# Kernel optimization log

Measured on AMD Instinct MI355X. Metric: run time of the kernel, lower is better.

Reference implementation:

```python
import jax, jax.numpy as jnp
import numpy as np

EPS = 1e-6
K_STEPS = 4
USE_GATING = True


def layer_norm(x, gamma, beta):
    mu = jnp.mean(x, axis=-1, keepdims=True)
    var = jnp.mean(jnp.square(x - mu), axis=-1, keepdims=True)
    return (x - mu) * jax.lax.rsqrt(var + EPS) * gamma + beta


def setup_inputs() -> dict:
    key = jax.random.key(0)
    B, L, D, H = 4, 4096, 2048, 8192
    ks = jax.random.split(key, 16)
    s = 0.02
    return {
        "x": jax.random.normal(ks[0], (B, L, D), dtype=jnp.float32),
        "in_gamma": jnp.ones((D,), jnp.float32),
        "in_beta": jnp.zeros((D,), jnp.float32),
        "agg_w": jax.random.normal(ks[1], (D, D), jnp.float32) * s,
        "agg_b": jnp.zeros((D,), jnp.float32),
        "pn_gamma": jnp.ones((D,), jnp.float32),
        "pn_beta": jnp.zeros((D,), jnp.float32),
        "d1_w": jax.random.normal(ks[2], (D, H), jnp.float32) * s,
        "d1_b": jnp.zeros((H,), jnp.float32),
        "d2_w": jax.random.normal(ks[3], (H, D), jnp.float32) * s,
        "d2_b": jnp.zeros((D,), jnp.float32),
        "bc_w": jax.random.normal(ks[4], (D, D), jnp.float32) * s,
        "bc_b": jnp.zeros((D,), jnp.float32),
        "gate_w": jax.random.normal(ks[5], (D, D), jnp.float32) * s,
        "gate_b": jnp.zeros((D,), jnp.float32),
        "out_gamma": jnp.ones((D,), jnp.float32),
        "out_beta": jnp.zeros((D,), jnp.float32),
    }


def reference(x, in_gamma, in_beta, agg_w, agg_b, pn_gamma, pn_beta,
              d1_w, d1_b, d2_w, d2_b, bc_w, bc_b, gate_w, gate_b,
              out_gamma, out_beta):
    # Input norm over the full sequence, then extract last-position summary.
    x_norm = layer_norm(x, in_gamma, in_beta)              # [B, L, D]
    thought = x_norm[:, -1, :] @ agg_w + agg_b             # [B, D]

    # Iterative pre-norm MLP thought refinement (fixed small k -> unrolled).
    for _ in range(K_STEPS):
        t = layer_norm(thought, pn_gamma, pn_beta)
        t = jax.nn.gelu(t @ d1_w + d1_b, approximate=False)
        thought = thought + (t @ d2_w + d2_b)

    # Broadcast refined thought back to every position.
    broadcast = (thought @ bc_w + bc_b)[:, None, :]        # [B, 1, D]

    if USE_GATING:
        gate = jax.nn.sigmoid(x @ gate_w + gate_b)         # [B, L, D]
        out = x + gate * broadcast
    else:
        out = x + broadcast
    return layer_norm(out, out_gamma, out_beta)
```

## Files before the change

kernel.cpp:

```cpp
#include <hip/hip_runtime.h>
#include <stdint.h>

typedef __attribute__((ext_vector_type(8))) short short8;
typedef __attribute__((ext_vector_type(4))) float f32x4;
typedef __attribute__((ext_vector_type(4))) unsigned short us4;

__device__ inline unsigned short f2bf(float f) {
    unsigned u = __float_as_uint(f);
    u = (u + 0x7FFFu + ((u >> 16) & 1u)) >> 16;
    return (unsigned short)u;
}

__device__ inline float bf2f(unsigned short u) {
    return __uint_as_float(((unsigned)u) << 16);
}

__device__ inline float gelu_f(float v) {
    return 0.5f * v * (1.0f + erff(v * 0.70710678118654752f));
}

__device__ inline void gload_lds16(const unsigned short* g, const unsigned short* l) {
    __builtin_amdgcn_global_load_lds(
        (const __attribute__((address_space(1))) unsigned int*)(g),
        (__attribute__((address_space(3))) unsigned int*)(l),
        16, 0, 0);
}

__global__ __launch_bounds__(256) void cvt_x_kernel(const float* __restrict__ in,
                                                    unsigned short* __restrict__ out, int n4) {
    int i = blockIdx.x * 256 + threadIdx.x;
    if (i >= n4) return;
    float4 v = reinterpret_cast<const float4*>(in)[i];
    us4 o = { f2bf(v.x), f2bf(v.y), f2bf(v.z), f2bf(v.w) };
    reinterpret_cast<us4*>(out)[i] = o;
}

__global__ __launch_bounds__(256) void transpose_w_kernel(const float* __restrict__ W,
                                                          unsigned short* __restrict__ WT,
                                                          int K, int N) {
    __shared__ float tile[32][33];
    int bn = blockIdx.x * 32;
    int bk = blockIdx.y * 32;
    int tx = threadIdx.x & 31;
    int ty = threadIdx.x >> 5;
#pragma unroll
    for (int j = 0; j < 32; j += 8)
        tile[ty + j][tx] = W[(long long)(bk + ty + j) * N + bn + tx];
    __syncthreads();
#pragma unroll
    for (int j = 0; j < 32; j += 8)
        WT[(long long)(bn + ty + j) * K + bk + tx] = f2bf(tile[tx][ty + j]);
}

__device__ inline void block_reduce2(float& s, float& q) {
#pragma unroll
    for (int o = 32; o > 0; o >>= 1) {
        s += __shfl_xor(s, o, 64);
        q += __shfl_xor(q, o, 64);
    }
    __shared__ float sh[8];
    __syncthreads();
    int w = threadIdx.x >> 6;
    if ((threadIdx.x & 63) == 0) { sh[w] = s; sh[4 + w] = q; }
    __syncthreads();
    s = (sh[0] + sh[1]) + (sh[2] + sh[3]);
    q = (sh[4] + sh[5]) + (sh[6] + sh[7]);
}

__global__ __launch_bounds__(256) void ln_rows_kernel(const float* __restrict__ in, long long in_stride,
                                                      float* __restrict__ out, long long out_stride,
                                                      const float* __restrict__ gamma,
                                                      const float* __restrict__ beta) {
    const float* p = in + (long long)blockIdx.x * in_stride;
    float* q = out + (long long)blockIdx.x * out_stride;
    int t = threadIdx.x;
    float4 a = reinterpret_cast<const float4*>(p)[t];
    float4 c = reinterpret_cast<const float4*>(p)[t + 256];
    float s  = (a.x + a.y) + (a.z + a.w) + (c.x + c.y) + (c.z + c.w);
    float ss = a.x*a.x + a.y*a.y + a.z*a.z + a.w*a.w
             + c.x*c.x + c.y*c.y + c.z*c.z + c.w*c.w;
    block_reduce2(s, ss);
    const float inv = 1.0f / 2048.0f;
    float mu = s * inv;
    float var = ss * inv - mu * mu;
    float rs = rsqrtf(var + 1e-6f);
    float4 g0 = reinterpret_cast<const float4*>(gamma)[t];
    float4 g1 = reinterpret_cast<const float4*>(gamma)[t + 256];
    float4 b0 = reinterpret_cast<const float4*>(beta)[t];
    float4 b1 = reinterpret_cast<const float4*>(beta)[t + 256];
    float4 o0, o1;
    o0.x = (a.x - mu) * rs * g0.x + b0.x;
    o0.y = (a.y - mu) * rs * g0.y + b0.y;
    o0.z = (a.z - mu) * rs * g0.z + b0.z;
    o0.w = (a.w - mu) * rs * g0.w + b0.w;
    o1.x = (c.x - mu) * rs * g1.x + b1.x;
    o1.y = (c.y - mu) * rs * g1.y + b1.y;
    o1.z = (c.z - mu) * rs * g1.z + b1.z;
    o1.w = (c.w - mu) * rs * g1.w + b1.w;
    reinterpret_cast<float4*>(q)[t] = o0;
    reinterpret_cast<float4*>(q)[t + 256] = o1;
}

template<int MODE>
__global__ __launch_bounds__(256) void gemv4f_kernel(const float* __restrict__ src, long long sstride,
                                                     const float* __restrict__ gamma,
                                                     const float* __restrict__ beta,
                                                     const float* __restrict__ W,
                                                     const float* __restrict__ bias,
                                                     float* __restrict__ out,
                                                     int K, int N, int KC) {
    __shared__ float sA[4][128];
    const int tid = threadIdx.x;
    const int k0 = blockIdx.y * KC;

    float mu[4], rsd[4];
    if (MODE == 1) {
#pragma unroll
        for (int r = 0; r < 4; ++r) {
            const float* p = src + r * sstride;
            float s = 0.f, q = 0.f;
            for (int k = tid; k < K; k += 256) { float v = p[k]; s += v; q += v * v; }
            block_reduce2(s, q);
            float m = s / K;
            mu[r] = m;
            rsd[r] = rsqrtf(q / K - m * m + 1e-6f);
        }
    }
    for (int idx = tid; idx < 4 * KC; idx += 256) {
        int r = idx / KC, k = idx - r * KC;
        float v = src[r * sstride + k0 + k];
        if (MODE == 1) v = (v - mu[r]) * rsd[r] * gamma[k0 + k] + beta[k0 + k];
        if (MODE == 2) v = gelu_f(v);
        sA[r][k] = v;
    }
    __syncthreads();

    const int n4 = blockIdx.x * 256 + tid;
    const int n = n4 * 4;
    const float4* W4 = reinterpret_cast<const float4*>(W);
    float4 a0 = {0.f, 0.f, 0.f, 0.f}, a1 = a0, a2 = a0, a3 = a0;
#pragma unroll 4
    for (int k = 0; k < KC; ++k) {
        float4 w = W4[((long long)(k0 + k) * N + n) >> 2];
        float c0 = sA[0][k], c1 = sA[1][k], c2 = sA[2][k], c3 = sA[3][k];
        a0.x = fmaf(c0, w.x, a0.x); a0.y = fmaf(c0, w.y, a0.y);
        a0.z = fmaf(c0, w.z, a0.z); a0.w = fmaf(c0, w.w, a0.w);
        a1.x = fmaf(c1, w.x, a1.x); a1.y = fmaf(c1, w.y, a1.y);
        a1.z = fmaf(c1, w.z, a1.z); a1.w = fmaf(c1, w.w, a1.w);
        a2.x = fmaf(c2, w.x, a2.x); a2.y = fmaf(c2, w.y, a2.y);
        a2.z = fmaf(c2, w.z, a2.z); a2.w = fmaf(c2, w.w, a2.w);
        a3.x = fmaf(c3, w.x, a3.x); a3.y = fmaf(c3, w.y, a3.y);
        a3.z = fmaf(c3, w.z, a3.z); a3.w = fmaf(c3, w.w, a3.w);
    }
    if (blockIdx.y == 0) {
        float4 b = reinterpret_cast<const float4*>(bias)[n4];
        a0.x += b.x; a0.y += b.y; a0.z += b.z; a0.w += b.w;
        a1.x += b.x; a1.y += b.y; a1.z += b.z; a1.w += b.w;
        a2.x += b.x; a2.y += b.y; a2.z += b.z; a2.w += b.w;
        a3.x += b.x; a3.y += b.y; a3.z += b.z; a3.w += b.w;
    }
    atomicAdd(&out[n + 0], a0.x); atomicAdd(&out[n + 1], a0.y);
    atomicAdd(&out[n + 2], a0.z); atomicAdd(&out[n + 3], a0.w);
    atomicAdd(&out[N + n + 0], a1.x); atomicAdd(&out[N + n + 1], a1.y);
    atomicAdd(&out[N + n + 2], a1.z); atomicAdd(&out[N + n + 3], a1.w);
    atomicAdd(&out[2 * N + n + 0], a2.x); atomicAdd(&out[2 * N + n + 1], a2.y);
    atomicAdd(&out[2 * N + n + 2], a2.z); atomicAdd(&out[2 * N + n + 3], a2.w);
    atomicAdd(&out[3 * N + n + 0], a3.x); atomicAdd(&out[3 * N + n + 1], a3.y);
    atomicAdd(&out[3 * N + n + 2], a3.z); atomicAdd(&out[3 * N + n + 3], a3.w);
}

#define BK 64
__global__ __launch_bounds__(512, 2) void gate_gemm_kernel(const unsigned short* __restrict__ A,
                                                           const unsigned short* __restrict__ BT,
                                                           const float* __restrict__ gate_b,
                                                           const float* __restrict__ bcast,
                                                           float* __restrict__ pre,
                                                           int M, int N, int K) {
    extern __shared__ unsigned short lds[];
    const int tid = threadIdx.x;
    const int lane = tid & 63;
    const int wave = tid >> 6;
    const int wm = wave >> 2;
    const int wn = wave & 3;
    const int bm0 = blockIdx.x * 256;
    const int bn0 = blockIdx.y * 256;
    const int NT = K / BK;

    const int ch0 = wave * 64 + lane;
    const int ch1 = 512 + wave * 64 + lane;
    const int r0 = ch0 >> 3, c0s = (ch0 & 7) ^ (r0 & 7);
    const int r1 = ch1 >> 3, c1s = (ch1 & 7) ^ (r1 & 7);
    const int srcoff0 = r0 * K + c0s * 8;
    const int srcoff1 = r1 * K + c1s * 8;
    const int ldso0 = ch0 * 8;
    const int ldso1 = ch1 * 8;

    const unsigned short* Abase = A + (long long)bm0 * K;
    const unsigned short* Bbase = BT + (long long)bn0 * K;

#define STAGE_A(buf, h, t)  do { \
        const unsigned short* g = Abase + (h) * 128 * K + (t) * BK; \
        const unsigned short* d = &lds[(buf) * 16384 + (h) * 8192]; \
        gload_lds16(g + srcoff0, d + ldso0); \
        gload_lds16(g + srcoff1, d + ldso1); } while (0)
#define STAGE_B(buf, h, t)  do { \
        const unsigned short* g = Bbase + (h) * 128 * K + (t) * BK; \
        const unsigned short* d = &lds[32768 + (buf) * 16384 + (h) * 8192]; \
        gload_lds16(g + srcoff0, d + ldso0); \
        gload_lds16(g + srcoff1, d + ldso1); } while (0)

    f32x4 acc[8][4];
#pragma unroll
    for (int i = 0; i < 8; ++i)
#pragma unroll
        for (int j = 0; j < 4; ++j)
#pragma unroll
            for (int r = 0; r < 4; ++r) acc[i][j][r] = 0.f;

    const int r16 = lane & 15, kq = lane >> 4;

    STAGE_A(0, 0, 0); STAGE_A(0, 1, 0);
    STAGE_B(0, 0, 0); STAGE_B(0, 1, 0);
    asm volatile("s_waitcnt vmcnt(0)" ::: "memory");
    __builtin_amdgcn_s_barrier();

    for (int t = 0; t < NT; ++t) {
        const int p = t & 1;
        const int u = t + 1;
        const int a_base = p * 16384 + wm * 8192;
        const int b_base = 32768 + p * 16384 + (wn >> 1) * 8192;

        if (u < NT) {
            STAGE_A(1 - p, 0, u); STAGE_A(1 - p, 1, u);
            STAGE_B(1 - p, 0, u); STAGE_B(1 - p, 1, u);
        }
        __builtin_amdgcn_sched_barrier(0);

        short8 bf[4][2];
#pragma unroll
        for (int ni = 0; ni < 4; ++ni) {
            const int rl = (wn & 1) * 64 + ni * 16 + r16;
#pragma unroll
            for (int kk = 0; kk < 2; ++kk)
                bf[ni][kk] = *reinterpret_cast<const short8*>(
                    &lds[b_base + rl * 64 + (((kk << 2) | kq) ^ (rl & 7)) * 8]);
        }
#pragma unroll
        for (int mh = 0; mh < 2; ++mh) {
            short8 af[4][2];
#pragma unroll
            for (int mi = 0; mi < 4; ++mi) {
                const int rl = mh * 64 + mi * 16 + r16;
#pragma unroll
                for (int kk = 0; kk < 2; ++kk)
                    af[mi][kk] = *reinterpret_cast<const short8*>(
                        &lds[a_base + rl * 64 + (((kk << 2) | kq) ^ (rl & 7)) * 8]);
            }
            __builtin_amdgcn_s_setprio(1);
#pragma unroll
            for (int mi = 0; mi < 4; ++mi)
#pragma unroll
                for (int ni = 0; ni < 4; ++ni)
#pragma unroll
                    for (int kk = 0; kk < 2; ++kk)
                        acc[mh * 4 + mi][ni] = __builtin_amdgcn_mfma_f32_16x16x32_bf16(
                            af[mi][kk], bf[ni][kk], acc[mh * 4 + mi][ni], 0, 0, 0);
            __builtin_amdgcn_s_setprio(0);
        }
        asm volatile("s_waitcnt vmcnt(0)" ::: "memory");
        __builtin_amdgcn_s_barrier();
    }

    const int bnum = bm0 >> 12;
    const float* bc_row = bcast + (long long)bnum * N;
#pragma unroll
    for (int mi = 0; mi < 8; ++mi) {
        const int row = bm0 + wm * 128 + mi * 16 + kq * 4;
#pragma unroll
        for (int ni = 0; ni < 4; ++ni) {
            const int col = bn0 + wn * 64 + ni * 16 + r16;
            const float gb = gate_b[col];
            const float bc = bc_row[col];
#pragma unroll
            for (int r = 0; r < 4; ++r) {
                const long long off = (long long)(row + r) * N + col;
                const float v = acc[mi][ni][r] + gb;
                const float g = 1.0f / (1.0f + __expf(-v));
                pre[off] = bf2f(A[off]) + g * bc;
            }
        }
    }
}
#undef STAGE_A
#undef STAGE_B

extern "C" void kernel_launch(void* const* d_in, const int* in_sizes, int n_in,
                              void* d_out, int out_size, void* d_ws, size_t ws_size,
                              hipStream_t stream) {
    const float* x         = (const float*)d_in[0];
    const float* in_gamma  = (const float*)d_in[1];
    const float* in_beta   = (const float*)d_in[2];
    const float* agg_w     = (const float*)d_in[3];
    const float* agg_b     = (const float*)d_in[4];
    const float* pn_gamma  = (const float*)d_in[5];
    const float* pn_beta   = (const float*)d_in[6];
    const float* d1_w      = (const float*)d_in[7];
    const float* d1_b      = (const float*)d_in[8];
    const float* d2_w      = (const float*)d_in[9];
    const float* d2_b      = (const float*)d_in[10];
    const float* bc_w      = (const float*)d_in[11];
    const float* bc_b      = (const float*)d_in[12];
    const float* gate_w    = (const float*)d_in[13];
    const float* gate_b    = (const float*)d_in[14];
    const float* out_gamma = (const float*)d_in[15];
    const float* out_beta  = (const float*)d_in[16];

    const int B = 4, L = 4096, D = 2048, H = 8192;
    const int M = B * L;
    float* out = (float*)d_out;

    char* ws = (char*)d_ws;
    unsigned short* xb  = (unsigned short*)ws;
    unsigned short* gwT = (unsigned short*)(ws + 67108864);
    float* tbuf  = (float*)(ws + 75497472);
    float* bcast = tbuf + 4 * D;
    float* hbuf0 = bcast + 4 * D;

    static bool attr_done = false;
    if (!attr_done) {
        hipFuncSetAttribute((const void*)gate_gemm_kernel,
                            hipFuncAttributeMaxDynamicSharedMemorySize, 131072);
        attr_done = true;
    }

    hipMemsetAsync(tbuf, 0, (4 * D + 4 * D + 4 * 4 * H) * sizeof(float), stream);

    gemv4f_kernel<1><<<dim3(D / 1024, 64), dim3(256), 0, stream>>>(
        x + (long long)(L - 1) * D, (long long)L * D, in_gamma, in_beta,
        agg_w, agg_b, tbuf, D, D, 32);

    for (int s = 0; s < 4; ++s) {
        float* hbuf = hbuf0 + s * 4 * H;
        gemv4f_kernel<1><<<dim3(H / 1024, 32), dim3(256), 0, stream>>>(
            tbuf, (long long)D, pn_gamma, pn_beta, d1_w, d1_b, hbuf, D, H, 64);
        gemv4f_kernel<2><<<dim3(D / 1024, 128), dim3(256), 0, stream>>>(
            hbuf, (long long)H, nullptr, nullptr, d2_w, d2_b, tbuf, H, D, 64);
    }
    gemv4f_kernel<0><<<dim3(D / 1024, 64), dim3(256), 0, stream>>>(
        tbuf, (long long)D, nullptr, nullptr, bc_w, bc_b, bcast, D, D, 32);

    cvt_x_kernel<<<dim3((M * D / 4) / 256), dim3(256), 0, stream>>>(x, xb, M * D / 4);
    transpose_w_kernel<<<dim3(D / 32, D / 32), dim3(256), 0, stream>>>(gate_w, gwT, D, D);

    gate_gemm_kernel<<<dim3(M / 256, D / 256), dim3(512), 131072, stream>>>(
        xb, gwT, gate_b, bcast, out, M, D, D);

    ln_rows_kernel<<<dim3(M), dim3(256), 0, stream>>>(
        out, (long long)D, out, (long long)D, out_gamma, out_beta);
}
```

Baseline: 525.8 us.

## Shrink gate GEMM tile to 128x128 and swap grid order for N-fastest traversal

Reduces the gate GEMM block tile from 256x256 to 128x128 with 512 threads. Each wave now computes a 64x32 sub-tile, LDS drops to 64KB, and launch bounds allow 4 blocks per CU. The grid is reordered so blockIdx.x walks N, which means consecutive blocks share the same A rows. The intent is higher occupancy and better latency hiding, paid for by lower arithmetic intensity per tile and more global and LDS traffic per FLOP.

```diff
diff --git a/kernel.cpp b/kernel.cpp
--- a/kernel.cpp
+++ b/kernel.cpp
@@ -170,7 +170,7 @@
 }
 
 #define BK 64
-__global__ __launch_bounds__(512, 2) void gate_gemm_kernel(const unsigned short* __restrict__ A,
+__global__ __launch_bounds__(512, 4) void gate_gemm_kernel(const unsigned short* __restrict__ A,
                                                            const unsigned short* __restrict__ BT,
                                                            const float* __restrict__ gate_b,
                                                            const float* __restrict__ bcast,
@@ -182,12 +182,11 @@
     const int wave = tid >> 6;
     const int wm = wave >> 2;
     const int wn = wave & 3;
-    const int bm0 = blockIdx.x * 256;
-    const int bn0 = blockIdx.y * 256;
+    const int bn0 = blockIdx.x * 128;
+    const int bm0 = blockIdx.y * 128;
     const int NT = K / BK;
 
-    const int ch0 = wave * 64 + lane;
-    const int ch1 = 512 + wave * 64 + lane;
+    const int ch0 = tid, ch1 = tid + 512;
     const int r0 = ch0 >> 3, c0s = (ch0 & 7) ^ (r0 & 7);
     const int r1 = ch1 >> 3, c1s = (ch1 & 7) ^ (r1 & 7);
     const int srcoff0 = r0 * K + c0s * 8;
@@ -198,75 +197,68 @@
     const unsigned short* Abase = A + (long long)bm0 * K;
     const unsigned short* Bbase = BT + (long long)bn0 * K;
 
-#define STAGE_A(buf, h, t)  do { \
-        const unsigned short* g = Abase + (h) * 128 * K + (t) * BK; \
-        const unsigned short* d = &lds[(buf) * 16384 + (h) * 8192]; \
+#define STAGE_A(buf, t)  do { \
+        const unsigned short* g = Abase + (t) * BK; \
+        const unsigned short* d = &lds[(buf) * 8192]; \
         gload_lds16(g + srcoff0, d + ldso0); \
         gload_lds16(g + srcoff1, d + ldso1); } while (0)
-#define STAGE_B(buf, h, t)  do { \
-        const unsigned short* g = Bbase + (h) * 128 * K + (t) * BK; \
-        const unsigned short* d = &lds[32768 + (buf) * 16384 + (h) * 8192]; \
+#define STAGE_B(buf, t)  do { \
+        const unsigned short* g = Bbase + (t) * BK; \
+        const unsigned short* d = &lds[16384 + (buf) * 8192]; \
         gload_lds16(g + srcoff0, d + ldso0); \
         gload_lds16(g + srcoff1, d + ldso1); } while (0)
 
-    f32x4 acc[8][4];
-#pragma unroll
-    for (int i = 0; i < 8; ++i)
-#pragma unroll
-        for (int j = 0; j < 4; ++j)
+    f32x4 acc[4][2];
+#pragma unroll
+    for (int i = 0; i < 4; ++i)
+#pragma unroll
+        for (int j = 0; j < 2; ++j)
 #pragma unroll
             for (int r = 0; r < 4; ++r) acc[i][j][r] = 0.f;
 
     const int r16 = lane & 15, kq = lane >> 4;
 
-    STAGE_A(0, 0, 0); STAGE_A(0, 1, 0);
-    STAGE_B(0, 0, 0); STAGE_B(0, 1, 0);
+    STAGE_A(0, 0); STAGE_B(0, 0);
     asm volatile("s_waitcnt vmcnt(0)" ::: "memory");
     __builtin_amdgcn_s_barrier();
 
     for (int t = 0; t < NT; ++t) {
         const int p = t & 1;
         const int u = t + 1;
-        const int a_base = p * 16384 + wm * 8192;
-        const int b_base = 32768 + p * 16384 + (wn >> 1) * 8192;
-
-        if (u < NT) {
-            STAGE_A(1 - p, 0, u); STAGE_A(1 - p, 1, u);
-            STAGE_B(1 - p, 0, u); STAGE_B(1 - p, 1, u);
-        }
+        const int a_base = p * 8192;
+        const int b_base = 16384 + p * 8192;
+
+        if (u < NT) { STAGE_A(1 - p, u); STAGE_B(1 - p, u); }
         __builtin_amdgcn_sched_barrier(0);
 
-        short8 bf[4][2];
-#pragma unroll
-        for (int ni = 0; ni < 4; ++ni) {
-            const int rl = (wn & 1) * 64 + ni * 16 + r16;
+        short8 bf[2][2];
+#pragma unroll
+        for (int ni = 0; ni < 2; ++ni) {
+            const int rl = wn * 32 + ni * 16 + r16;
 #pragma unroll
             for (int kk = 0; kk < 2; ++kk)
                 bf[ni][kk] = *reinterpret_cast<const short8*>(
                     &lds[b_base + rl * 64 + (((kk << 2) | kq) ^ (rl & 7)) * 8]);
         }
-#pragma unroll
-        for (int mh = 0; mh < 2; ++mh) {
-            short8 af[4][2];
-#pragma unroll
-            for (int mi = 0; mi < 4; ++mi) {
-                const int rl = mh * 64 + mi * 16 + r16;
+        short8 af[4][2];
+#pragma unroll
+        for (int mi = 0; mi < 4; ++mi) {
+            const int rl = wm * 64 + mi * 16 + r16;
+#pragma unroll
+            for (int kk = 0; kk < 2; ++kk)
+                af[mi][kk] = *reinterpret_cast<const short8*>(
+                    &lds[a_base + rl * 64 + (((kk << 2) | kq) ^ (rl & 7)) * 8]);
+        }
+        __builtin_amdgcn_s_setprio(1);
+#pragma unroll
+        for (int mi = 0; mi < 4; ++mi)
+#pragma unroll
+            for (int ni = 0; ni < 2; ++ni)
 #pragma unroll
                 for (int kk = 0; kk < 2; ++kk)
-                    af[mi][kk] = *reinterpret_cast<const short8*>(
-                        &lds[a_base + rl * 64 + (((kk << 2) | kq) ^ (rl & 7)) * 8]);
-            }
-            __builtin_amdgcn_s_setprio(1);
-#pragma unroll
-            for (int mi = 0; mi < 4; ++mi)
-#pragma unroll
-                for (int ni = 0; ni < 4; ++ni)
-#pragma unroll
-                    for (int kk = 0; kk < 2; ++kk)
-                        acc[mh * 4 + mi][ni] = __builtin_amdgcn_mfma_f32_16x16x32_bf16(
-                            af[mi][kk], bf[ni][kk], acc[mh * 4 + mi][ni], 0, 0, 0);
-            __builtin_amdgcn_s_setprio(0);
-        }
+                    acc[mi][ni] = __builtin_amdgcn_mfma_f32_16x16x32_bf16(
+                        af[mi][kk], bf[ni][kk], acc[mi][ni], 0, 0, 0);
+        __builtin_amdgcn_s_setprio(0);
         asm volatile("s_waitcnt vmcnt(0)" ::: "memory");
         __builtin_amdgcn_s_barrier();
     }
@@ -274,11 +266,11 @@
     const int bnum = bm0 >> 12;
     const float* bc_row = bcast + (long long)bnum * N;
 #pragma unroll
-    for (int mi = 0; mi < 8; ++mi) {
-        const int row = bm0 + wm * 128 + mi * 16 + kq * 4;
-#pragma unroll
-        for (int ni = 0; ni < 4; ++ni) {
-            const int col = bn0 + wn * 64 + ni * 16 + r16;
+    for (int mi = 0; mi < 4; ++mi) {
+        const int row = bm0 + wm * 64 + mi * 16 + kq * 4;
+#pragma unroll
+        for (int ni = 0; ni < 2; ++ni) {
+            const int col = bn0 + wn * 32 + ni * 16 + r16;
             const float gb = gate_b[col];
             const float bc = bc_row[col];
 #pragma unroll
@@ -329,7 +321,7 @@
     static bool attr_done = false;
     if (!attr_done) {
         hipFuncSetAttribute((const void*)gate_gemm_kernel,
-                            hipFuncAttributeMaxDynamicSharedMemorySize, 131072);
+                            hipFuncAttributeMaxDynamicSharedMemorySize, 65536);
         attr_done = true;
     }
 
@@ -352,7 +344,7 @@
     cvt_x_kernel<<<dim3((M * D / 4) / 256), dim3(256), 0, stream>>>(x, xb, M * D / 4);
     transpose_w_kernel<<<dim3(D / 32, D / 32), dim3(256), 0, stream>>>(gate_w, gwT, D, D);
 
-    gate_gemm_kernel<<<dim3(M / 256, D / 256), dim3(512), 131072, stream>>>(
+    gate_gemm_kernel<<<dim3(D / 128, M / 128), dim3(512), 65536, stream>>>(
         xb, gwT, gate_b, bcast, out, M, D, D);
 
     ln_rows_kernel<<<dim3(M), dim3(256), 0, stream>>>(
```

Measured after the change: 539.0 us. 2.5% more time.
